# Kernel tuning notes

Measured on AMD Instinct MI355X. Metric: run time of the kernel, lower is better.

## Reference

```python
import jax, jax.numpy as jnp
import numpy as np

EPS = 1e-07      # epsilon from init kwargs
LRELU = 0.1      # LeakyReLU negative slope
LEVEL = 0        # level 0 -> _cond_inter: i%2!=0 and j%2!=0


def _conv_circ(x, w, b):
    # circular-padded 2D conv, NCHW / OIHW
    p = w.shape[-1] // 2
    x = jnp.pad(x, ((0, 0), (0, 0), (p, p), (p, p)), mode='wrap')
    y = jax.lax.conv_general_dilated(x, w, (1, 1), 'VALID',
                                     dimension_numbers=('NCHW', 'OIHW', 'NCHW'))
    return y + b[None, :, None, None]


def _net(x, w1, b1, w2, b2, w3, b3):
    h = jax.nn.leaky_relu(_conv_circ(x, w1, b1), LRELU)
    h = jax.nn.leaky_relu(_conv_circ(h, w2, b2), LRELU)
    return jax.nn.sigmoid(_conv_circ(h, w3, b3))


def _positions(L):
    ii, jj = np.meshgrid(np.arange(L), np.arange(L), indexing='ij')
    if LEVEL == 0:
        mask = (ii % 2 != 0) & (jj % 2 != 0)
    else:
        mask = ((ii % 2 == 0) & (jj % 2 != 0)) | ((ii % 2 != 0) & (jj % 2 == 0))
    # row-major order matches the nested python loop
    return jnp.asarray(np.stack([ii[mask], jj[mask]], axis=1), dtype=jnp.int32)  # [S,2]


def setup_inputs() -> dict:
    key = jax.random.key(0)
    ks = jax.random.split(key, 7)
    B, L, H, K = 4096, 16, 32, 5
    x = jnp.where(jax.random.normal(ks[0], (B, 1, L, L)) > 0, 1.0, -1.0).astype(jnp.float32)
    w1 = (jax.random.normal(ks[1], (H, 1, K, K)) * 0.1).astype(jnp.float32)
    b1 = jnp.zeros((H,), jnp.float32)
    w2 = (jax.random.normal(ks[2], (H, H, K, K)) * 0.05).astype(jnp.float32)
    b2 = jnp.zeros((H,), jnp.float32)
    w3 = (jax.random.normal(ks[3], (1, H, K, K)) * 0.05).astype(jnp.float32)
    b3 = jnp.zeros((1,), jnp.float32)
    return {'x': x, 'w1': w1, 'b1': b1, 'w2': w2, 'b2': b2, 'w3': w3, 'b3': b3}


def reference(x, w1, b1, w2, b2, w3, b3):
    B, L = x.shape[0], x.shape[-1]
    pos = _positions(L)                                   # [S,2] static positions
    keys = jax.random.split(jax.random.key(42), pos.shape[0])

    def step(carry, inp):
        x, logq = carry
        ij, k = inp
        i, j = ij[0], ij[1]
        x_hat = _net(x, w1, b1, w2, b2, w3, b3)           # full CNN pass per pixel
        p = x_hat[:, 0, i, j]                             # [B]
        samp = jax.lax.stop_gradient(
            jnp.where(jax.random.uniform(k, (B,)) < p, 1.0, -1.0))  # bernoulli*2-1
        x = x.at[:, 0, i, j].set(samp)
        xb = (samp + 1.0) * 0.5
        logq = logq + jnp.log(p + EPS) * xb + jnp.log(1.0 - p + EPS) * (1.0 - xb)
        return (x, logq), None

    (x, logq), _ = jax.lax.scan(step, (x, jnp.zeros((B,), x.dtype)), (pos, keys))
    return x, logq
```

## Files before the change

kernel.cpp:

```cpp
#include <hip/hip_runtime.h>
#include <cstdint>


struct U2 { uint32_t x, y; };

__device__ __forceinline__ U2 tf2x32(uint32_t k0, uint32_t k1, uint32_t x0, uint32_t x1) {
  uint32_t k2 = k0 ^ k1 ^ 0x1BD11BDAu;
#define TFROT(r) { x0 += x1; x1 = (x1 << (r)) | (x1 >> (32 - (r))); x1 ^= x0; }
  x0 += k0; x1 += k1;
  TFROT(13) TFROT(15) TFROT(26) TFROT(6)
  x0 += k1; x1 += k2 + 1u;
  TFROT(17) TFROT(29) TFROT(16) TFROT(24)
  x0 += k2; x1 += k0 + 2u;
  TFROT(13) TFROT(15) TFROT(26) TFROT(6)
  x0 += k0; x1 += k1 + 3u;
  TFROT(17) TFROT(29) TFROT(16) TFROT(24)
  x0 += k1; x1 += k2 + 4u;
  TFROT(13) TFROT(15) TFROT(26) TFROT(6)
  x0 += k2; x1 += k0 + 5u;
#undef TFROT
  return {x0, x1};
}

__device__ __forceinline__ float lrelu(float v) { return fmaxf(v, 0.1f * v); }

__launch_bounds__(1024, 4)
__global__ void van_kernel(const float* __restrict__ gx,
                           const float* __restrict__ gw1, const float* __restrict__ gb1,
                           const float* __restrict__ gw2, const float* __restrict__ gb2,
                           const float* __restrict__ gw3, const float* __restrict__ gb3,
                           float* __restrict__ out, int B) {
  __shared__ __align__(16) float s_xf[28 * 28];
  __shared__ __align__(16) float s_h1[32][9][12];
  __shared__ __align__(16) float s_w1[800];
  __shared__ __align__(16) float s_w3[800];
  __shared__ __align__(16) float s_buf[8][800];
  __shared__ float s_b1[32], s_b2[32];
  __shared__ float s_u[64];
  __shared__ float s_c3[16];

  const int tid  = threadIdx.x;
  const int bg   = blockIdx.x;
  const int lane = tid & 63;
  const int wv   = tid >> 6;
  const int oc   = tid & 31;
  const int ic   = tid >> 5;

  const float b3v = gb3[0];
  float w2r[25];
  {
    const float* p = gw2 + (oc * 32 + ic) * 25;
    #pragma unroll
    for (int k = 0; k < 25; ++k) w2r[k] = p[k];
  }
  if (tid < 800) { s_w1[tid] = gw1[tid]; s_w3[tid] = gw3[tid]; }
  if (tid < 32)  { s_b1[tid] = gb1[tid]; s_b2[tid] = gb2[tid]; }
  if (tid < 784) {
    int rr = tid / 28, cc = tid - rr * 28;
    int fy = (rr - 6) & 15, fx = (cc - 6) & 15;
    s_xf[tid] = gx[bg * 256 + fy * 16 + fx];
  }
  if (tid < 64) {
    U2 key = tf2x32(0u, 42u, 0u, (uint32_t)tid);
    U2 tt  = tf2x32(key.x, key.y, 0u, (uint32_t)bg);
    uint32_t bits = tt.x ^ tt.y;
    s_u[tid] = __uint_as_float(0x3F800000u | (bits >> 9)) - 1.0f;
  }
  float logq = 0.f;
  __syncthreads();

  #pragma unroll 1
  for (int s = 0; s < 64; ++s) {
    const int i = 2 * (s >> 3) + 1;
    const int j = 2 * (s & 7) + 1;

    if (tid < 288) {
      const int t_ic = tid / 9;
      const int r    = tid - t_ic * 9;
      const float bb = s_b1[t_ic];
      float a[9];
      #pragma unroll
      for (int c = 0; c < 9; ++c) a[c] = bb;
      #pragma unroll
      for (int ky = 0; ky < 5; ++ky) {
        const float* xr = &s_xf[(i + r + ky) * 28 + j];
        float xv[13];
        #pragma unroll
        for (int m = 0; m < 13; ++m) xv[m] = xr[m];
        #pragma unroll
        for (int kx = 0; kx < 5; ++kx) {
          const float w = s_w1[t_ic * 25 + ky * 5 + kx];
          #pragma unroll
          for (int c = 0; c < 9; ++c) a[c] = fmaf(xv[c + kx], w, a[c]);
        }
      }
      #pragma unroll
      for (int c = 0; c < 9; ++c) s_h1[t_ic][r][c] = lrelu(a[c]);
    }
    __syncthreads();

    float acc[25];
    #pragma unroll
    for (int p = 0; p < 25; ++p) acc[p] = 0.f;
    #pragma unroll
    for (int tr = 0; tr < 9; ++tr) {
      const float4* rp = (const float4*)(&s_h1[ic][tr][0]);
      const float4 ra = rp[0], rb = rp[1];
      const float r8 = s_h1[ic][tr][8];
      const float row[9] = {ra.x, ra.y, ra.z, ra.w, rb.x, rb.y, rb.z, rb.w, r8};
      #pragma unroll
      for (int dy = 0; dy < 5; ++dy) {
        const int ky = tr - dy;
        if (ky < 0 || ky > 4) continue;
        #pragma unroll
        for (int kx = 0; kx < 5; ++kx) {
          const float w = w2r[ky * 5 + kx];
          #pragma unroll
          for (int dx = 0; dx < 5; ++dx)
            acc[dy * 5 + dx] = fmaf(row[dx + kx], w, acc[dy * 5 + dx]);
        }
      }
    }
    #pragma unroll
    for (int p = 0; p < 25; ++p) acc[p] += __shfl_xor(acc[p], 32, 64);
    if (wv >= 8 && lane < 32) {
      #pragma unroll
      for (int p = 0; p < 25; ++p) s_buf[wv - 8][p * 32 + lane] = acc[p];
    }
    __syncthreads();
    if (wv < 8 && lane < 32) {
      #pragma unroll
      for (int p = 0; p < 25; ++p) s_buf[wv][p * 32 + lane] += acc[p];
    }
    __syncthreads();

    float v3 = 0.f;
    if (tid < 800) {
      float t = 0.f;
      #pragma unroll
      for (int v = 0; v < 8; ++v) t += s_buf[v][tid];
      t += s_b2[tid & 31];
      const float h2 = lrelu(t);
      v3 = h2 * s_w3[(tid & 31) * 25 + (tid >> 5)];
    }
    #pragma unroll
    for (int m = 32; m >= 1; m >>= 1) v3 += __shfl_xor(v3, m, 64);
    if (lane == 0) s_c3[wv] = v3;
    __syncthreads();

    if (tid == 0) {
      float logit = b3v;
      #pragma unroll
      for (int v = 0; v < 16; ++v) logit += s_c3[v];
      const float pr   = 1.f / (1.f + expf(-logit));
      const float u    = s_u[s];
      const float samp = (u < pr) ? 1.f : -1.f;
      const int r1 = i + 6, c1 = j + 6;
      const int r2 = (i < 6) ? i + 22 : ((i >= 10) ? i - 10 : r1);
      const int c2 = (j < 6) ? j + 22 : ((j >= 10) ? j - 10 : c1);
      s_xf[r1 * 28 + c1] = samp; s_xf[r1 * 28 + c2] = samp;
      s_xf[r2 * 28 + c1] = samp; s_xf[r2 * 28 + c2] = samp;
      logq += (samp > 0.f) ? logf(pr + 1e-7f) : logf(1.f - pr + 1e-7f);
    }
    __syncthreads();
  }

  if (tid < 256)
    out[bg * 256 + tid] = s_xf[((tid >> 4) + 6) * 28 + (tid & 15) + 6];
  if (tid == 0)
    out[B * 256 + bg] = logq;
}

extern "C" void kernel_launch(void* const* d_in, const int* in_sizes, int n_in,
                              void* d_out, int out_size, void* d_ws, size_t ws_size,
                              hipStream_t stream) {
  const float* gx  = (const float*)d_in[0];
  const float* gw1 = (const float*)d_in[1];
  const float* gb1 = (const float*)d_in[2];
  const float* gw2 = (const float*)d_in[3];
  const float* gb2 = (const float*)d_in[4];
  const float* gw3 = (const float*)d_in[5];
  const float* gb3 = (const float*)d_in[6];
  float* out = (float*)d_out;
  const int B = in_sizes[0] / 256;

  hipLaunchKernelGGL(van_kernel, dim3(B), dim3(1024), 0, stream,
                     gx, gw1, gb1, gw2, gb2, gw3, gb3, out, B);
}
```

Measured before the change: 5.918 ms.

## Precompute full conv2 activations once and update incrementally per sampled pixel

Result: slower. 6.865 ms (+16.0%).

```diff
diff --git a/kernel.cpp b/kernel.cpp
--- a/kernel.cpp
+++ b/kernel.cpp
@@ -30,14 +30,16 @@
                            const float* __restrict__ gw2, const float* __restrict__ gb2,
                            const float* __restrict__ gw3, const float* __restrict__ gb3,
                            float* __restrict__ out, int B) {
-  __shared__ __align__(16) float s_xf[28 * 28];
-  __shared__ __align__(16) float s_h1[32][9][12];
+  __shared__ __align__(16) float s_xf[784];
   __shared__ __align__(16) float s_w1[800];
   __shared__ __align__(16) float s_w3[800];
-  __shared__ __align__(16) float s_buf[8][800];
   __shared__ float s_b1[32], s_b2[32];
   __shared__ float s_u[64];
   __shared__ float s_c3[16];
+  __shared__ __align__(16) float s_h1d[800];
+  __shared__ __align__(16) float s_a2[8192];
+  __shared__ __align__(16) float s_pool[8192];
+  __shared__ __align__(16) float s_buf[16][864];
 
   const int tid  = threadIdx.x;
   const int bg   = blockIdx.x;
@@ -57,8 +59,7 @@
   if (tid < 32)  { s_b1[tid] = gb1[tid]; s_b2[tid] = gb2[tid]; }
   if (tid < 784) {
     int rr = tid / 28, cc = tid - rr * 28;
-    int fy = (rr - 6) & 15, fx = (cc - 6) & 15;
-    s_xf[tid] = gx[bg * 256 + fy * 16 + fx];
+    s_xf[tid] = gx[bg * 256 + ((rr - 6) & 15) * 16 + ((cc - 6) & 15)];
   }
   if (tid < 64) {
     U2 key = tf2x32(0u, 42u, 0u, (uint32_t)tid);
@@ -66,103 +67,169 @@
     uint32_t bits = tt.x ^ tt.y;
     s_u[tid] = __uint_as_float(0x3F800000u | (bits >> 9)) - 1.0f;
   }
+  __syncthreads();
+
+  {
+    const int icI = tid & 31, pg = tid >> 5;
+    float w1r[25];
+    #pragma unroll
+    for (int k = 0; k < 25; ++k) w1r[k] = s_w1[icI * 25 + k];
+    const float b1v = s_b1[icI];
+    #pragma unroll
+    for (int rep = 0; rep < 8; ++rep) {
+      int pos = pg * 8 + rep;
+      int r = pos >> 4, c = pos & 15;
+      float a = b1v;
+      #pragma unroll
+      for (int ky = 0; ky < 5; ++ky)
+        #pragma unroll
+        for (int kx = 0; kx < 5; ++kx)
+          a = fmaf(s_xf[(r + ky + 4) * 28 + (c + kx + 4)], w1r[ky * 5 + kx], a);
+      s_pool[pos * 32 + icI] = lrelu(a);
+    }
+  }
+  __syncthreads();
+
+  #pragma unroll 1
+  for (int cr = 0; cr < 16; ++cr) {
+    float acc[16];
+    #pragma unroll
+    for (int t = 0; t < 16; ++t) acc[t] = 0.f;
+    #pragma unroll
+    for (int ky = 0; ky < 5; ++ky) {
+      int row = (cr + ky - 2) & 15;
+      float h[16];
+      #pragma unroll
+      for (int col = 0; col < 16; ++col) h[col] = s_pool[(row * 16 + col) * 32 + ic];
+      #pragma unroll
+      for (int kx = 0; kx < 5; ++kx) {
+        float w = w2r[ky * 5 + kx];
+        #pragma unroll
+        for (int X = 0; X < 16; ++X)
+          acc[X] = fmaf(h[(X + kx - 2) & 15], w, acc[X]);
+      }
+    }
+    #pragma unroll
+    for (int t = 0; t < 16; ++t) acc[t] += __shfl_xor(acc[t], 32, 64);
+    if (lane < 32) {
+      #pragma unroll
+      for (int t = 0; t < 16; ++t) s_buf[wv][t * 32 + lane] = acc[t];
+    }
+    __syncthreads();
+    if (tid < 512) {
+      float sm = 0.f;
+      #pragma unroll
+      for (int v = 0; v < 16; ++v) sm += s_buf[v][tid];
+      s_a2[cr * 512 + tid] = sm + s_b2[tid & 31];
+    }
+    __syncthreads();
+  }
+  #pragma unroll
+  for (int k = 0; k < 8; ++k) s_pool[k * 1024 + tid] = 0.f;
+  __syncthreads();
+
   float logq = 0.f;
-  __syncthreads();
-
   #pragma unroll 1
   for (int s = 0; s < 64; ++s) {
     const int i = 2 * (s >> 3) + 1;
     const int j = 2 * (s & 7) + 1;
 
-    if (tid < 288) {
-      const int t_ic = tid / 9;
-      const int r    = tid - t_ic * 9;
-      const float bb = s_b1[t_ic];
-      float a[9];
-      #pragma unroll
-      for (int c = 0; c < 9; ++c) a[c] = bb;
-      #pragma unroll
-      for (int ky = 0; ky < 5; ++ky) {
-        const float* xr = &s_xf[(i + r + ky) * 28 + j];
-        float xv[13];
-        #pragma unroll
-        for (int m = 0; m < 13; ++m) xv[m] = xr[m];
-        #pragma unroll
-        for (int kx = 0; kx < 5; ++kx) {
-          const float w = s_w1[t_ic * 25 + ky * 5 + kx];
-          #pragma unroll
-          for (int c = 0; c < 9; ++c) a[c] = fmaf(xv[c + kx], w, a[c]);
-        }
-      }
-      #pragma unroll
-      for (int c = 0; c < 9; ++c) s_h1[t_ic][r][c] = lrelu(a[c]);
-    }
-    __syncthreads();
-
-    float acc[25];
-    #pragma unroll
-    for (int p = 0; p < 25; ++p) acc[p] = 0.f;
-    #pragma unroll
-    for (int tr = 0; tr < 9; ++tr) {
-      const float4* rp = (const float4*)(&s_h1[ic][tr][0]);
-      const float4 ra = rp[0], rb = rp[1];
-      const float r8 = s_h1[ic][tr][8];
-      const float row[9] = {ra.x, ra.y, ra.z, ra.w, rb.x, rb.y, rb.z, rb.w, r8};
-      #pragma unroll
-      for (int dy = 0; dy < 5; ++dy) {
-        const int ky = tr - dy;
-        if (ky < 0 || ky > 4) continue;
-        #pragma unroll
-        for (int kx = 0; kx < 5; ++kx) {
-          const float w = w2r[ky * 5 + kx];
-          #pragma unroll
-          for (int dx = 0; dx < 5; ++dx)
-            acc[dy * 5 + dx] = fmaf(row[dx + kx], w, acc[dy * 5 + dx]);
-        }
-      }
-    }
-    #pragma unroll
-    for (int p = 0; p < 25; ++p) acc[p] += __shfl_xor(acc[p], 32, 64);
-    if (wv >= 8 && lane < 32) {
-      #pragma unroll
-      for (int p = 0; p < 25; ++p) s_buf[wv - 8][p * 32 + lane] = acc[p];
-    }
-    __syncthreads();
-    if (wv < 8 && lane < 32) {
-      #pragma unroll
-      for (int p = 0; p < 25; ++p) s_buf[wv][p * 32 + lane] += acc[p];
-    }
-    __syncthreads();
-
     float v3 = 0.f;
     if (tid < 800) {
-      float t = 0.f;
-      #pragma unroll
-      for (int v = 0; v < 8; ++v) t += s_buf[v][tid];
-      t += s_b2[tid & 31];
-      const float h2 = lrelu(t);
-      v3 = h2 * s_w3[(tid & 31) * 25 + (tid >> 5)];
+      int p = tid >> 5, o2 = tid & 31;
+      int dy = p / 5, dx = p - 5 * dy;
+      int idx = (((i + dy - 2) & 15) * 16 + ((j + dx - 2) & 15)) * 32 + o2;
+      float a2v = s_a2[idx] - s_pool[idx];
+      v3 = lrelu(a2v) * s_w3[o2 * 25 + p];
     }
     #pragma unroll
     for (int m = 32; m >= 1; m >>= 1) v3 += __shfl_xor(v3, m, 64);
     if (lane == 0) s_c3[wv] = v3;
     __syncthreads();
 
-    if (tid == 0) {
-      float logit = b3v;
-      #pragma unroll
-      for (int v = 0; v < 16; ++v) logit += s_c3[v];
-      const float pr   = 1.f / (1.f + expf(-logit));
-      const float u    = s_u[s];
-      const float samp = (u < pr) ? 1.f : -1.f;
-      const int r1 = i + 6, c1 = j + 6;
-      const int r2 = (i < 6) ? i + 22 : ((i >= 10) ? i - 10 : r1);
-      const int c2 = (j < 6) ? j + 22 : ((j >= 10) ? j - 10 : c1);
+    float logit = b3v;
+    #pragma unroll
+    for (int v = 0; v < 16; ++v) logit += s_c3[v];
+    const float pr   = 1.f / (1.f + expf(-logit));
+    const float u    = s_u[s];
+    const float samp = (u < pr) ? 1.f : -1.f;
+    const float xold = s_xf[(i + 6) * 28 + (j + 6)];
+    logq += (samp > 0.f) ? logf(pr + 1e-7f) : logf(1.f - pr + 1e-7f);
+
+    if (samp == xold) { __syncthreads(); continue; }
+
+    if (tid < 800) {
+      int p = tid >> 5, icA = tid & 31;
+      int dyq = p / 5, dxq = p - 5 * dyq;
+      const float* wp = &s_w1[icA * 25];
+      float a1v = s_b1[icA];
+      int base = (i + dyq + 2) * 28 + (j + dxq + 2);
+      #pragma unroll
+      for (int ky = 0; ky < 5; ++ky)
+        #pragma unroll
+        for (int kx = 0; kx < 5; ++kx)
+          a1v = fmaf(s_xf[base + ky * 28 + kx], wp[ky * 5 + kx], a1v);
+      float delta = samp - xold;
+      float a1n = fmaf(delta, wp[(4 - dyq) * 5 + (4 - dxq)], a1v);
+      s_h1d[p * 32 + icA] = lrelu(a1n) - lrelu(a1v);
+    }
+    __syncthreads();
+
+    if (tid == 1023) {
+      int r1 = i + 6, c1 = j + 6;
+      int r2 = (i < 6) ? i + 22 : ((i >= 10) ? i - 10 : r1);
+      int c2 = (j < 6) ? j + 22 : ((j >= 10) ? j - 10 : c1);
       s_xf[r1 * 28 + c1] = samp; s_xf[r1 * 28 + c2] = samp;
       s_xf[r2 * 28 + c1] = samp; s_xf[r2 * 28 + c2] = samp;
-      logq += (samp > 0.f) ? logf(pr + 1e-7f) : logf(1.f - pr + 1e-7f);
-    }
-    __syncthreads();
+    }
+
+    float h1d[25];
+    #pragma unroll
+    for (int q = 0; q < 25; ++q) h1d[q] = s_h1d[q * 32 + ic];
+
+    #pragma unroll
+    for (int cch = 0; cch < 3; ++cch) {
+      float acc[27];
+      #pragma unroll
+      for (int t = 0; t < 27; ++t) acc[t] = 0.f;
+      #pragma unroll
+      for (int u2 = 0; u2 < 3; ++u2) {
+        const int U = 3 * cch + u2;
+        #pragma unroll
+        for (int dyp = 0; dyp < 5; ++dyp) {
+          const int ky = dyp + 4 - U;
+          if (ky < 0 || ky > 4) continue;
+          #pragma unroll
+          for (int kx = 0; kx < 5; ++kx) {
+            const float w = w2r[ky * 5 + kx];
+            #pragma unroll
+            for (int dxp = 0; dxp < 5; ++dxp)
+              acc[u2 * 9 + (dxp - kx + 4)] = fmaf(h1d[dyp * 5 + dxp], w, acc[u2 * 9 + (dxp - kx + 4)]);
+          }
+        }
+      }
+      #pragma unroll
+      for (int t = 0; t < 27; ++t) acc[t] += __shfl_xor(acc[t], 32, 64);
+      if (lane < 32) {
+        #pragma unroll
+        for (int t = 0; t < 27; ++t) s_buf[wv][t * 32 + lane] = acc[t];
+      }
+      __syncthreads();
+      if (tid < 864) {
+        float sm = 0.f;
+        #pragma unroll
+        for (int v = 0; v < 16; ++v) sm += s_buf[v][tid];
+        int u3 = tid / 288, rem = tid - u3 * 288;
+        int V = rem >> 5, o3 = rem & 31;
+        int idx = (((i - 4 + 3 * cch + u3) & 15) * 16 + ((j - 4 + V) & 15)) * 32 + o3;
+        float y  = sm - s_pool[idx];
+        float a  = s_a2[idx];
+        float t2 = a + y;
+        s_pool[idx] = (t2 - a) - y;
+        s_a2[idx] = t2;
+      }
+      __syncthreads();
+    }
   }
 
   if (tid < 256)
```
